# Performance work log

Measured on AMD Instinct MI355X. Metric: run time of the kernel, lower is better.

## Reference

```python
import jax, jax.numpy as jnp
import numpy as np

B, LQ, LK, D, H = 4, 1024, 2048, 1024, 16
DH = D // H  # 64
EPS = 1e-6
ROPE_BASE = 10000.0


def _rms_norm(x, w):
    # RMSNorm over last dim (d_head)
    var = jnp.mean(jnp.square(x), axis=-1, keepdims=True)
    return x * jax.lax.rsqrt(var + EPS) * w


def _rope(x, pos):
    # x: [B,H,L,dh], pos: [L] int. Half-split rotation.
    half = x.shape[-1] // 2
    inv_freq = ROPE_BASE ** (-jnp.arange(0, half, dtype=jnp.float32) / half)
    ang = pos.astype(jnp.float32)[:, None] * inv_freq  # [L, half]
    cos, sin = jnp.cos(ang), jnp.sin(ang)              # [L, half]
    x1, x2 = x[..., :half], x[..., half:]
    return jnp.concatenate([x1 * cos - x2 * sin, x1 * sin + x2 * cos], axis=-1)


def setup_inputs() -> dict:
    key = jax.random.key(0)
    ks = jax.random.split(key, 7)
    s = 1.0 / np.sqrt(D)
    return {
        "queries": jax.random.normal(ks[0], (B, LQ, D), jnp.float32),
        "kv": jax.random.normal(ks[1], (B, LK, D), jnp.float32),
        "wq": jax.random.normal(ks[2], (D, D), jnp.float32) * s,
        "wkv": jax.random.normal(ks[3], (2 * D, D), jnp.float32) * s,
        "wo": jax.random.normal(ks[4], (D, D), jnp.float32) * s,
        "q_norm_w": jnp.ones((DH,), jnp.float32),
        "k_norm_w": jnp.ones((DH,), jnp.float32),
        "pos_q": jnp.arange(LQ, dtype=jnp.int32),
        "pos_k": jnp.arange(LK, dtype=jnp.int32),
    }


def reference(queries, kv, wq, wkv, wo, q_norm_w, k_norm_w, pos_q, pos_k):
    b, lq, d = queries.shape
    lk = kv.shape[1]
    scale = DH ** -0.5
    # projections (torch Linear: x @ W.T)
    q = (queries @ wq.T).reshape(b, lq, H, DH).transpose(0, 2, 1, 3)  # [B,H,Lq,dh]
    kvp = (kv @ wkv.T).reshape(b, lk, H, 2 * DH).transpose(0, 2, 1, 3)
    k, v = kvp[..., :DH], kvp[..., DH:]                               # [B,H,Lk,dh]
    q = _rms_norm(q, q_norm_w)
    k = _rms_norm(k, k_norm_w)
    q = _rope(q, pos_q)
    k = _rope(k, pos_k)
    scores = jnp.einsum("bhqd,bhkd->bhqk", q, k) * scale
    attn = jax.nn.softmax(scores, axis=-1)
    y = jnp.einsum("bhqk,bhkd->bhqd", attn, v)        # [B,H,Lq,dh]
    y = y.transpose(0, 2, 1, 3).reshape(b, lq, d)     # [B,Lq,D]
    return y @ wo.T
```

## Files before the change

kernel.cpp:

```cpp
#include <hip/hip_runtime.h>
#include <stdint.h>

typedef unsigned short u16;
typedef u16 u16x8 __attribute__((ext_vector_type(8)));
typedef u16 u16x4 __attribute__((ext_vector_type(4)));
typedef short s16x8 __attribute__((ext_vector_type(8)));
typedef float f32x4 __attribute__((ext_vector_type(4)));

#define B_ 4
#define LQ_ 1024
#define LK_ 2048
#define D_ 1024
#define H_ 16
#define DH_ 64
#define QSCL 0.1803368801111204f
#define L2_10000 13.287712379549449f

__device__ __forceinline__ u16 f2bf(float x) {
  uint32_t u = __float_as_uint(x);
  u += 0x7FFFu + ((u >> 16) & 1u);
  return (u16)(u >> 16);
}
__device__ __forceinline__ float bf2f(u16 h) {
  return __uint_as_float(((uint32_t)h) << 16);
}
__device__ __forceinline__ uint32_t cvtpk(float lo, float hi) {
  uint32_t r;
  asm("v_cvt_pk_bf16_f32 %0, %1, %2" : "=v"(r) : "v"(lo), "v"(hi));
  return r;
}
__device__ __forceinline__ float exp2fast(float x) {
  float r;
  asm("v_exp_f32 %0, %1" : "=v"(r) : "v"(x));
  return r;
}

__global__ __launch_bounds__(256) void castw_k(const float* __restrict__ src,
                                               u16* __restrict__ dst, int n) {
  int i = (blockIdx.x * 256 + threadIdx.x) * 4;
  if (i >= n) return;
  float4 v = *(const float4*)(src + i);
  ushort4 o;
  o.x = f2bf(v.x); o.y = f2bf(v.y); o.z = f2bf(v.z); o.w = f2bf(v.w);
  *(ushort4*)(dst + i) = o;
}

__global__ __launch_bounds__(256) void gemm_bt(const u16* __restrict__ A,
                                               const u16* __restrict__ Bm,
                                               float* __restrict__ C,
                                               int N) {
  __shared__ __align__(16) u16 As[2][128 * 32];
  __shared__ __align__(16) u16 Bs[2][128 * 32];
  const int tid = threadIdx.x;
  const int lane = tid & 63;
  const int wid = tid >> 6;
  const int m0 = blockIdx.x * 128;
  const int n0 = blockIdx.y * 128;
  const int slice = 1024 / gridDim.z;
  const int kStart = blockIdx.z * slice;
  const int NT = slice >> 5;
  C += (size_t)blockIdx.z * (size_t)gridDim.x * 128 * N;
  const int wr = (wid >> 1) * 64;
  const int wc = (wid & 1) * 64;
  const int fr = lane & 15;
  const int fq = lane >> 4;
  const int srow = lane >> 2;
  const int schunk = lane & 3;

  f32x4 zero = {0.f, 0.f, 0.f, 0.f};
  f32x4 acc[4][4];
  for (int i = 0; i < 4; i++)
    for (int j = 0; j < 4; j++) acc[i][j] = zero;

  const int r0 = wid * 32;
  const u16* gA = A + (size_t)(m0 + r0 + srow) * 1024 + schunk * 8;
  const u16* gB = Bm + (size_t)(n0 + r0 + srow) * 1024 + schunk * 8;

  auto stage = [&](int buf, int k0) {
    u16* lA = &As[buf][r0 * 32];
    u16* lB = &Bs[buf][r0 * 32];
    __builtin_amdgcn_global_load_lds(
        (const __attribute__((address_space(1))) void*)(gA + k0),
        (__attribute__((address_space(3))) void*)(lA), 16, 0, 0);
    __builtin_amdgcn_global_load_lds(
        (const __attribute__((address_space(1))) void*)(gA + k0 + (size_t)16 * 1024),
        (__attribute__((address_space(3))) void*)(lA + 16 * 32), 16, 0, 0);
    __builtin_amdgcn_global_load_lds(
        (const __attribute__((address_space(1))) void*)(gB + k0),
        (__attribute__((address_space(3))) void*)(lB), 16, 0, 0);
    __builtin_amdgcn_global_load_lds(
        (const __attribute__((address_space(1))) void*)(gB + k0 + (size_t)16 * 1024),
        (__attribute__((address_space(3))) void*)(lB + 16 * 32), 16, 0, 0);
  };

  stage(0, kStart);
  stage(1, kStart + 32);
  asm volatile("s_waitcnt vmcnt(4)" ::: "memory");
  __builtin_amdgcn_s_barrier();

  for (int t = 0; t < NT; t++) {
    const int cur = t & 1;
    s16x8 af[4], bf[4];
#pragma unroll
    for (int mi = 0; mi < 4; mi++)
      af[mi] = *(const s16x8*)&As[cur][(wr + mi * 16 + fr) * 32 + fq * 8];
#pragma unroll
    for (int ni = 0; ni < 4; ni++)
      bf[ni] = *(const s16x8*)&Bs[cur][(wc + ni * 16 + fr) * 32 + fq * 8];
#pragma unroll
    for (int mi = 0; mi < 4; mi++)
#pragma unroll
      for (int ni = 0; ni < 4; ni++)
        acc[mi][ni] = __builtin_amdgcn_mfma_f32_16x16x32_bf16(af[mi], bf[ni],
                                                              acc[mi][ni], 0, 0, 0);
    __builtin_amdgcn_s_barrier();
    if (t + 2 < NT) {
      stage(cur, kStart + (t + 2) * 32);
      asm volatile("s_waitcnt vmcnt(4)" ::: "memory");
    } else {
      asm volatile("s_waitcnt vmcnt(0)" ::: "memory");
    }
    __builtin_amdgcn_s_barrier();
  }
#pragma unroll
  for (int mi = 0; mi < 4; mi++) {
#pragma unroll
    for (int ni = 0; ni < 4; ni++) {
      int row = m0 + wr + mi * 16 + fq * 4;
      int col = n0 + wc + ni * 16 + fr;
#pragma unroll
      for (int r = 0; r < 4; r++) C[(size_t)(row + r) * N + col] = acc[mi][ni][r];
    }
  }
}

#define BAR8 asm volatile("s_barrier" ::: "memory")
__global__ __launch_bounds__(512, 2) void gemm_bt256(const u16* __restrict__ A,
                                                     const u16* __restrict__ Bm,
                                                     u16* __restrict__ C) {
  __shared__ __align__(16) u16 lds[65536];
  const int N = 2048;
  const int tid = threadIdx.x;
  const int lane = tid & 63;
  const int w = tid >> 6;
  const int wr = w >> 2;
  const int wc = w & 3;
  const int fr = lane & 15;
  const int fq = lane >> 4;
  const int nwg = gridDim.x;
  const int cpx = nwg >> 3;
  const int bid = blockIdx.x;
  const int swz = (bid & 7) * cpx + (bid >> 3);
  const int nbn = N >> 8;
  const int bm = swz / nbn, bn = swz % nbn;
  const int gm0 = bm * 256, gn0 = bn * 256;
  const int NT = 16;

  f32x4 zero = {0.f, 0.f, 0.f, 0.f};
  f32x4 acc[8][4];
#pragma unroll
  for (int i = 0; i < 8; i++)
#pragma unroll
    for (int j = 0; j < 4; j++) acc[i][j] = zero;

  auto stage = [&](int buf, int t, int s) {
    int q = (s & 3) * 512 + tid;
    int row = q >> 3, p = q & 7;
    int l = p ^ (row & 7);
    const u16* src = (s < 4)
        ? A + (size_t)(gm0 + row) * 1024 + (t << 6) + l * 8
        : Bm + (size_t)(gn0 + row) * 1024 + (t << 6) + l * 8;
    u16* dst = &lds[buf * 32768 + ((s < 4) ? 0 : 16384) + ((s & 3) * 512 + w * 64) * 8];
    __builtin_amdgcn_global_load_lds(
        (const __attribute__((address_space(1))) void*)src,
        (__attribute__((address_space(3))) void*)dst, 16, 0, 0);
  };
  auto rdA = [&](int buf, int mi, int kk) -> s16x8 {
    int row = wr * 128 + mi * 16 + fr;
    int l = (kk * 4 + fq) ^ (fr & 7);
    return *(const s16x8*)&lds[buf * 32768 + row * 64 + l * 8];
  };
  auto rdB = [&](int buf, int ni, int kk) -> s16x8 {
    int row = wc * 64 + ni * 16 + fr;
    int l = (kk * 4 + fq) ^ (fr & 7);
    return *(const s16x8*)&lds[buf * 32768 + 16384 + row * 64 + l * 8];
  };

  s16x8 af[4][2], bf[4][2];

#pragma unroll
  for (int s = 4; s < 8; s++) stage(0, 0, s);
#pragma unroll
  for (int s = 0; s < 4; s++) stage(0, 0, s);
#pragma unroll
  for (int s = 4; s < 8; s++) stage(1, 1, s);
#pragma unroll
  for (int s = 0; s < 4; s++) stage(1, 1, s);
  asm volatile("s_waitcnt vmcnt(8)" ::: "memory");
  BAR8;

  for (int t = 0; t < NT; t++) {
    const int cur = t & 1;
    const bool st2 = (t + 2 < NT);
#pragma unroll
    for (int mi = 0; mi < 4; mi++)
#pragma unroll
      for (int kk = 0; kk < 2; kk++) af[mi][kk] = rdA(cur, mi, kk);
#pragma unroll
    for (int ni = 0; ni < 2; ni++)
#pragma unroll
      for (int kk = 0; kk < 2; kk++) bf[ni][kk] = rdB(cur, ni, kk);
    BAR8;
    __builtin_amdgcn_s_setprio(1);
#pragma unroll
    for (int mi = 0; mi < 4; mi++)
#pragma unroll
      for (int ni = 0; ni < 2; ni++)
#pragma unroll
        for (int kk = 0; kk < 2; kk++)
          acc[mi][ni] = __builtin_amdgcn_mfma_f32_16x16x32_bf16(af[mi][kk], bf[ni][kk],
                                                                acc[mi][ni], 0, 0, 0);
    __builtin_amdgcn_s_setprio(0);
    BAR8;
#pragma unroll
    for (int ni = 2; ni < 4; ni++)
#pragma unroll
      for (int kk = 0; kk < 2; kk++) bf[ni][kk] = rdB(cur, ni, kk);
    BAR8;
    __builtin_amdgcn_s_setprio(1);
#pragma unroll
    for (int mi = 0; mi < 4; mi++)
#pragma unroll
      for (int ni = 2; ni < 4; ni++)
#pragma unroll
        for (int kk = 0; kk < 2; kk++)
          acc[mi][ni] = __builtin_amdgcn_mfma_f32_16x16x32_bf16(af[mi][kk], bf[ni][kk],
                                                                acc[mi][ni], 0, 0, 0);
    __builtin_amdgcn_s_setprio(0);
    BAR8;
#pragma unroll
    for (int mi = 0; mi < 4; mi++)
#pragma unroll
      for (int kk = 0; kk < 2; kk++) af[mi][kk] = rdA(cur, mi + 4, kk);
    if (st2) {
#pragma unroll
      for (int s = 4; s < 8; s++) stage(cur, t + 2, s);
    }
    BAR8;
    __builtin_amdgcn_s_setprio(1);
#pragma unroll
    for (int mi = 0; mi < 4; mi++)
#pragma unroll
      for (int ni = 2; ni < 4; ni++)
#pragma unroll
        for (int kk = 0; kk < 2; kk++)
          acc[mi + 4][ni] = __builtin_amdgcn_mfma_f32_16x16x32_bf16(
              af[mi][kk], bf[ni][kk], acc[mi + 4][ni], 0, 0, 0);
    __builtin_amdgcn_s_setprio(0);
    BAR8;
    if (st2) {
#pragma unroll
      for (int s = 0; s < 4; s++) stage(cur, t + 2, s);
      asm volatile("s_waitcnt vmcnt(8)" ::: "memory");
    } else {
      asm volatile("s_waitcnt vmcnt(0)" ::: "memory");
    }
    BAR8;
    __builtin_amdgcn_s_setprio(1);
#pragma unroll
    for (int mi = 0; mi < 4; mi++)
#pragma unroll
      for (int ni = 0; ni < 2; ni++)
#pragma unroll
        for (int kk = 0; kk < 2; kk++)
          acc[mi + 4][ni] = __builtin_amdgcn_mfma_f32_16x16x32_bf16(
              af[mi][kk], bf[ni][kk], acc[mi + 4][ni], 0, 0, 0);
    __builtin_amdgcn_s_setprio(0);
    BAR8;
  }
#pragma unroll
  for (int mi = 0; mi < 8; mi++) {
#pragma unroll
    for (int ni = 0; ni < 4; ni++) {
      int row = gm0 + wr * 128 + mi * 16 + fq * 4;
      int col = gn0 + wc * 64 + ni * 16 + fr;
#pragma unroll
      for (int r = 0; r < 4; r++) C[(size_t)(row + r) * N + col] = f2bf(acc[mi][ni][r]);
    }
  }
}

__global__ __launch_bounds__(256) void norm_rope_q(const float* __restrict__ src,
                                                   size_t partStride,
                                                   const float* __restrict__ w,
                                                   const int* __restrict__ pos,
                                                   u16* __restrict__ dst) {
  int wid = threadIdx.x >> 6;
  int lane = threadIdx.x & 63;
  int g = blockIdx.x * 4 + wid;
  int h = g & 15;
  int bl = g >> 4;
  int b = bl >> 10;
  int l = bl & 1023;
  size_t idx = (size_t)bl * 1024 + h * 64 + lane;
  float x = src[idx] + src[partStride + idx];
  float ss = x * x;
#pragma unroll
  for (int m = 1; m < 64; m <<= 1) ss += __shfl_xor(ss, m, 64);
  float xn = x * rsqrtf(ss * (1.0f / 64.0f) + 1e-6f) * w[lane];
  float p = __shfl_xor(xn, 32, 64);
  int j = lane & 31;
  float freq = exp2fast(-(float)j * (L2_10000 / 32.f));
  float ang = (float)pos[l] * freq;
  float c = cosf(ang), s = sinf(ang);
  float o = (lane < 32) ? (xn * c - p * s) : (p * s + xn * c);
  dst[((size_t)(b * 16 + h) * 1024 + l) * 64 + lane] = f2bf(o * QSCL);
}

__global__ __launch_bounds__(256) void norm_rope_kv(const u16* __restrict__ src,
                                                    const float* __restrict__ w,
                                                    const int* __restrict__ pos,
                                                    u16* __restrict__ dst) {
  int wid = threadIdx.x >> 6;
  int lane = threadIdx.x & 63;
  int g = blockIdx.x * 4 + wid;
  int h = g & 15;
  int bl = g >> 4;
  int b = bl >> 11;
  int l = bl & 2047;
  float x = bf2f(src[(size_t)bl * 2048 + h * 128 + lane]);
  float ss = x * x;
#pragma unroll
  for (int m = 1; m < 64; m <<= 1) ss += __shfl_xor(ss, m, 64);
  float xn = x * rsqrtf(ss * (1.0f / 64.0f) + 1e-6f) * w[lane];
  float p = __shfl_xor(xn, 32, 64);
  int j = lane & 31;
  float freq = exp2fast(-(float)j * (L2_10000 / 32.f));
  float ang = (float)pos[l] * freq;
  float c = cosf(ang), s = sinf(ang);
  float o = (lane < 32) ? (xn * c - p * s) : (p * s + xn * c);
  dst[((size_t)(b * 16 + h) * 2048 + l) * 64 + lane] = f2bf(o);
}

__global__ __launch_bounds__(256) void reduce2_k(const float* __restrict__ p,
                                                 float* __restrict__ out, int n) {
  int i = (blockIdx.x * 256 + threadIdx.x) * 4;
  if (i >= n) return;
  float4 a = *(const float4*)(p + i);
  float4 b = *(const float4*)(p + (size_t)n + i);
  float4 r = make_float4(a.x + b.x, a.y + b.y, a.z + b.z, a.w + b.w);
  *(float4*)(out + i) = r;
}

__global__ __launch_bounds__(256) void vtrans_k(const u16* __restrict__ kvp,
                                                u16* __restrict__ vt) {
  __shared__ u16 tile[64][66];
  int kt = blockIdx.x & 31;
  int bh = blockIdx.x >> 5;
  int h = bh & 15;
  int b = bh >> 4;
  int c = threadIdx.x & 63;
  int r4 = threadIdx.x >> 6;
  const u16* src = kvp + ((size_t)(b * LK_ + kt * 64)) * 2048 + h * 128 + 64;
#pragma unroll
  for (int p = 0; p < 16; p++) {
    int lk = p * 4 + r4;
    tile[lk][c] = src[(size_t)lk * 2048 + c];
  }
  __syncthreads();
  u16* dst = vt + (size_t)bh * 64 * LK_ + kt * 64;
#pragma unroll
  for (int p = 0; p < 16; p++) {
    int dh = p * 4 + r4;
    dst[(size_t)dh * LK_ + c] = tile[c][dh];
  }
}

__global__ __launch_bounds__(256) void flash_k(const u16* __restrict__ qb,
                                               const u16* __restrict__ kb,
                                               const u16* __restrict__ vb,
                                               u16* __restrict__ y1) {
  __shared__ __align__(16) u16 Ks[2][64][64];
  __shared__ __align__(16) u16 Vs[2][64][64];
  const int tid = threadIdx.x;
  const int lane = tid & 63;
  const int wid = tid >> 6;
  const int fr = lane & 15;
  const int fq = lane >> 4;
  int bid = blockIdx.x;
  int vbid = (bid & 7) * 64 + (bid >> 3);
  int qt = vbid & 7;
  int bh = vbid >> 3;
  const u16* qbase = qb + ((size_t)bh * LQ_ + qt * 128 + wid * 32) * 64;
  const u16* kbase = kb + (size_t)bh * LK_ * 64;
  const u16* vbase = vb + (size_t)bh * 64 * LK_;
  s16x8 qf0a = *(const s16x8*)(qbase + (size_t)fr * 64 + fq * 8);
  s16x8 qf1a = *(const s16x8*)(qbase + (size_t)fr * 64 + 32 + fq * 8);
  s16x8 qf0b = *(const s16x8*)(qbase + (size_t)(16 + fr) * 64 + fq * 8);
  s16x8 qf1b = *(const s16x8*)(qbase + (size_t)(16 + fr) * 64 + 32 + fq * 8);
  float mrunA = -1e30f, lrunA = 0.f;
  float mrunB = -1e30f, lrunB = 0.f;
  f32x4 zero = {0.f, 0.f, 0.f, 0.f};
  f32x4 yaccA[4], yaccB[4];
#pragma unroll
  for (int ni = 0; ni < 4; ni++) { yaccA[ni] = zero; yaccB[ni] = zero; }
  const int srow = tid >> 3;
  const int schunk = tid & 7;
  const int c2 = schunk >> 2, c1 = (schunk >> 1) & 1, c0 = schunk & 1;
  const int vg1 = 4 * c2 + 2 * c0;
  const int voff = 4 * c1;

  auto kaddr = [&](int bufi, int row) -> u16* {
    return &Ks[bufi][row][(schunk ^ (row & 7)) << 3];
  };
  auto stageV = [&](int bufi, int row, u16x8 v) {
    u16x4 lo4 = __builtin_shufflevector(v, v, 0, 1, 2, 3);
    u16x4 hi4 = __builtin_shufflevector(v, v, 4, 5, 6, 7);
    *(u16x4*)&Vs[bufi][row][((vg1 ^ (row & 7)) << 3) + voff] = lo4;
    *(u16x4*)&Vs[bufi][row][(((vg1 + 1) ^ (row & 7)) << 3) + voff] = hi4;
  };
  auto qk2 = [&](int bufi, f32x4 (&sA)[4], f32x4 (&sB)[4]) {
#pragma unroll
    for (int ni = 0; ni < 4; ni++) { sA[ni] = zero; sB[ni] = zero; }
#pragma unroll
    for (int ni = 0; ni < 4; ni++) {
      int row = ni * 16 + fr;
      s16x8 kf0 = *(const s16x8*)&Ks[bufi][row][(fq ^ (fr & 7)) << 3];
      s16x8 kf1 = *(const s16x8*)&Ks[bufi][row][((4 + fq) ^ (fr & 7)) << 3];
      sA[ni] = __builtin_amdgcn_mfma_f32_16x16x32_bf16(kf0, qf0a, sA[ni], 0, 0, 0);
      sA[ni] = __builtin_amdgcn_mfma_f32_16x16x32_bf16(kf1, qf1a, sA[ni], 0, 0, 0);
      sB[ni] = __builtin_amdgcn_mfma_f32_16x16x32_bf16(kf0, qf0b, sB[ni], 0, 0, 0);
      sB[ni] = __builtin_amdgcn_mfma_f32_16x16x32_bf16(kf1, qf1b, sB[ni], 0, 0, 0);
    }
  };
  auto softmax = [&](f32x4 (&sp)[4], float& mrun, float& lrun, f32x4 (&yacc)[4]) {
    float m0 = fmaxf(fmaxf(sp[0][0], sp[0][1]), sp[0][2]);
    float m1 = fmaxf(fmaxf(sp[0][3], sp[1][0]), sp[1][1]);
    float m2 = fmaxf(fmaxf(sp[1][2], sp[1][3]), sp[2][0]);
    float m3 = fmaxf(fmaxf(sp[2][1], sp[2][2]), sp[2][3]);
    float m4 = fmaxf(fmaxf(sp[3][0], sp[3][1]), sp[3][2]);
    float mx = fmaxf(fmaxf(fmaxf(m0, m1), m2), fmaxf(fmaxf(m3, m4), sp[3][3]));
    mx = fmaxf(mx, __shfl_xor(mx, 16, 64));
    mx = fmaxf(mx, __shfl_xor(mx, 32, 64));
    bool skip = __all(mx <= mrun + 10.0f);
    float ts = 0.f;
    if (!skip) {
      float mn = fmaxf(mrun, mx);
      float alpha = exp2fast(mrun - mn);
      mrun = mn;
      float va[4];
#pragma unroll
      for (int r = 0; r < 4; r++) va[r] = __shfl(alpha, fq * 4 + r, 64);
#pragma unroll
      for (int ni = 0; ni < 4; ni++)
#pragma unroll
        for (int r = 0; r < 4; r++) yacc[ni][r] *= va[r];
      lrun *= alpha;
    }
#pragma unroll
    for (int ni = 0; ni < 4; ni++)
#pragma unroll
      for (int r = 0; r < 4; r++) {
        float pv = exp2fast(sp[ni][r] - mrun);
        sp[ni][r] = pv;
        ts += pv;
      }
    ts += __shfl_xor(ts, 16, 64);
    ts += __shfl_xor(ts, 32, 64);
    lrun += ts;
  };

  const int NT = LK_ / 64;
  f32x4 spA[4], spB[4], snA[4], snB[4];

  {
    u16x8 k0 = *(const u16x8*)(kbase + (size_t)srow * 64 + schunk * 8);
    u16x8 k1 = *(const u16x8*)(kbase + (size_t)(srow + 32) * 64 + schunk * 8);
    u16x8 v0 = *(const u16x8*)(vbase + (size_t)srow * LK_ + schunk * 8);
    u16x8 v1 = *(const u16x8*)(vbase + (size_t)(srow + 32) * LK_ + schunk * 8);
    *(u16x8*)kaddr(0, srow) = k0;
    *(u16x8*)kaddr(0, srow + 32) = k1;
    stageV(0, srow, v0);
    stageV(0, srow + 32, v1);
    __syncthreads();
    u16x8 ka = *(const u16x8*)(kbase + (size_t)(64 + srow) * 64 + schunk * 8);
    u16x8 kb2 = *(const u16x8*)(kbase + (size_t)(64 + srow + 32) * 64 + schunk * 8);
    u16x8 va = *(const u16x8*)(vbase + (size_t)srow * LK_ + 64 + schunk * 8);
    u16x8 vb2 = *(const u16x8*)(vbase + (size_t)(srow + 32) * LK_ + 64 + schunk * 8);
    *(u16x8*)kaddr(1, srow) = ka;
    *(u16x8*)kaddr(1, srow + 32) = kb2;
    stageV(1, srow, va);
    stageV(1, srow + 32, vb2);
    qk2(0, spA, spB);
    __syncthreads();
  }

  for (int t = 0; t < NT; t++) {
    const int cur = t & 1;
    const bool st2 = (t + 2 < NT);
    u16x8 kr0, kr1, vr0, vr1;
    if (st2) {
      int kt = (t + 2) * 64;
      kr0 = *(const u16x8*)(kbase + (size_t)(kt + srow) * 64 + schunk * 8);
      kr1 = *(const u16x8*)(kbase + (size_t)(kt + srow + 32) * 64 + schunk * 8);
      vr0 = *(const u16x8*)(vbase + (size_t)srow * LK_ + kt + schunk * 8);
      vr1 = *(const u16x8*)(vbase + (size_t)(srow + 32) * LK_ + kt + schunk * 8);
    }
    if (t + 1 < NT) qk2(cur ^ 1, snA, snB);
    softmax(spA, mrunA, lrunA, yaccA);
    softmax(spB, mrunB, lrunB, yaccB);
#pragma unroll
    for (int s2 = 0; s2 < 2; s2++) {
      union { uint32_t u[4]; s16x8 v8; } puA, puB;
      puA.u[0] = cvtpk(spA[2 * s2][0], spA[2 * s2][1]);
      puA.u[1] = cvtpk(spA[2 * s2][2], spA[2 * s2][3]);
      puA.u[2] = cvtpk(spA[2 * s2 + 1][0], spA[2 * s2 + 1][1]);
      puA.u[3] = cvtpk(spA[2 * s2 + 1][2], spA[2 * s2 + 1][3]);
      puB.u[0] = cvtpk(spB[2 * s2][0], spB[2 * s2][1]);
      puB.u[1] = cvtpk(spB[2 * s2][2], spB[2 * s2][3]);
      puB.u[2] = cvtpk(spB[2 * s2 + 1][0], spB[2 * s2 + 1][1]);
      puB.u[3] = cvtpk(spB[2 * s2 + 1][2], spB[2 * s2 + 1][3]);
#pragma unroll
      for (int ni = 0; ni < 4; ni++) {
        int row = ni * 16 + fr;
        s16x8 vf = *(const s16x8*)&Vs[cur][row][(((4 * s2 + fq) ^ (fr & 7)) << 3)];
        yaccA[ni] = __builtin_amdgcn_mfma_f32_16x16x32_bf16(puA.v8, vf, yaccA[ni], 0, 0, 0);
        yaccB[ni] = __builtin_amdgcn_mfma_f32_16x16x32_bf16(puB.v8, vf, yaccB[ni], 0, 0, 0);
      }
    }
    __syncthreads();
    if (st2) {
      *(u16x8*)kaddr(cur, srow) = kr0;
      *(u16x8*)kaddr(cur, srow + 32) = kr1;
      stageV(cur, srow, vr0);
      stageV(cur, srow + 32, vr1);
    }
    __syncthreads();
#pragma unroll
    for (int ni = 0; ni < 4; ni++) { spA[ni] = snA[ni]; spB[ni] = snB[ni]; }
  }
  int b = bh >> 4, h = bh & 15;
  float lrA[4], lrB[4];
#pragma unroll
  for (int r = 0; r < 4; r++) {
    lrA[r] = __shfl(lrunA, fq * 4 + r, 64);
    lrB[r] = __shfl(lrunB, fq * 4 + r, 64);
  }
  u16* yoA = y1 + ((size_t)(b * LQ_ + qt * 128 + wid * 32 + fq * 4)) * 1024 + h * 64;
  u16* yoB = yoA + (size_t)16 * 1024;
#pragma unroll
  for (int ni = 0; ni < 4; ni++) {
#pragma unroll
    for (int r = 0; r < 4; r++) {
      yoA[(size_t)r * 1024 + ni * 16 + fr] = f2bf(yaccA[ni][r] / lrA[r]);
      yoB[(size_t)r * 1024 + ni * 16 + fr] = f2bf(yaccB[ni][r] / lrB[r]);
    }
  }
}

extern "C" void kernel_launch(void* const* d_in, const int* in_sizes, int n_in,
                              void* d_out, int out_size, void* d_ws, size_t ws_size,
                              hipStream_t stream) {
  (void)in_sizes; (void)n_in; (void)out_size;
  const float* queries = (const float*)d_in[0];
  const float* kv = (const float*)d_in[1];
  const float* wq = (const float*)d_in[2];
  const float* wkv = (const float*)d_in[3];
  const float* wo = (const float*)d_in[4];
  const float* qnw = (const float*)d_in[5];
  const float* knw = (const float*)d_in[6];
  const int* pos_q = (const int*)d_in[7];
  const int* pos_k = (const int*)d_in[8];
  float* out = (float*)d_out;

  char* ws = (char*)d_ws;
  size_t off = 0;
  auto alloc = [&](size_t sz) { void* p = ws + off; off += sz; return p; };
  u16* Aq1 = (u16*)alloc((size_t)4096 * 1024 * 2);
  u16* Wqh = (u16*)alloc((size_t)1024 * 1024 * 2);
  u16* Akv1 = (u16*)alloc((size_t)8192 * 1024 * 2);
  u16* Wkvh = (u16*)alloc((size_t)2048 * 1024 * 2);
  u16* Woh = (u16*)alloc((size_t)1024 * 1024 * 2);
  u16* KVp = (u16*)alloc((size_t)8192 * 2048 * 2);
  u16* Qb = (u16*)alloc((size_t)64 * 1024 * 64 * 2);
  u16* Kb = (u16*)alloc((size_t)64 * 2048 * 64 * 2);
  u16* Vt = (u16*)alloc((size_t)64 * 2048 * 64 * 2);
  u16* Y1 = (u16*)alloc((size_t)4096 * 1024 * 2);
  float* Part = (float*)alloc((size_t)2 * 4096 * 1024 * 4);
  if (off > ws_size) return;

  const size_t PSTRIDE = (size_t)4096 * 1024;

  castw_k<<<4096 * 1024 / 1024, 256, 0, stream>>>(queries, Aq1, 4096 * 1024);
  castw_k<<<1024 * 1024 / 1024, 256, 0, stream>>>(wq, Wqh, 1024 * 1024);
  castw_k<<<8192 * 1024 / 1024, 256, 0, stream>>>(kv, Akv1, 8192 * 1024);
  castw_k<<<2048 * 1024 / 1024, 256, 0, stream>>>(wkv, Wkvh, 2048 * 1024);
  castw_k<<<1024 * 1024 / 1024, 256, 0, stream>>>(wo, Woh, 1024 * 1024);
  gemm_bt256<<<(8192 / 256) * (2048 / 256), 512, 0, stream>>>(Akv1, Wkvh, KVp);
  gemm_bt<<<dim3(4096 / 128, 1024 / 128, 2), 256, 0, stream>>>(Aq1, Wqh, Part, 1024);
  norm_rope_q<<<4096 * 16 / 4, 256, 0, stream>>>(Part, PSTRIDE, qnw, pos_q, Qb);
  norm_rope_kv<<<8192 * 16 / 4, 256, 0, stream>>>(KVp, knw, pos_k, Kb);
  vtrans_k<<<64 * 32, 256, 0, stream>>>(KVp, Vt);
  flash_k<<<64 * 8, 256, 0, stream>>>(Qb, Kb, Vt, Y1);
  gemm_bt<<<dim3(4096 / 128, 1024 / 128, 2), 256, 0, stream>>>(Y1, Woh, Part, 1024);
  reduce2_k<<<4096, 256, 0, stream>>>(Part, out, 4096 * 1024);
}
```

Before: 207.3 us.

## Fuse K norm-rope with V transpose; compute softmax row sums via MFMA

Merges the K RMSNorm+RoPE kernel and the V transpose kernel into a single launch that processes one 64-row tile of K and V per block. This removes one launch and lets both parts share the block's indexing. In the flash kernel, the per-row softmax denominator is no longer built from exp sums and cross-lane shuffles. Instead, an extra MFMA multiplies the bf16 probabilities by a ones vector, which adds MFMA work but removes VALU adds and shuffles; the denominator now sums bf16-rounded probabilities rather than fp32 ones.

```diff
diff --git a/kernel.cpp b/kernel.cpp
--- a/kernel.cpp
+++ b/kernel.cpp
@@ -317,29 +317,49 @@
   dst[((size_t)(b * 16 + h) * 1024 + l) * 64 + lane] = f2bf(o * QSCL);
 }
 
-__global__ __launch_bounds__(256) void norm_rope_kv(const u16* __restrict__ src,
-                                                    const float* __restrict__ w,
-                                                    const int* __restrict__ pos,
-                                                    u16* __restrict__ dst) {
-  int wid = threadIdx.x >> 6;
-  int lane = threadIdx.x & 63;
-  int g = blockIdx.x * 4 + wid;
-  int h = g & 15;
-  int bl = g >> 4;
-  int b = bl >> 11;
-  int l = bl & 2047;
-  float x = bf2f(src[(size_t)bl * 2048 + h * 128 + lane]);
-  float ss = x * x;
-#pragma unroll
-  for (int m = 1; m < 64; m <<= 1) ss += __shfl_xor(ss, m, 64);
-  float xn = x * rsqrtf(ss * (1.0f / 64.0f) + 1e-6f) * w[lane];
-  float p = __shfl_xor(xn, 32, 64);
-  int j = lane & 31;
-  float freq = exp2fast(-(float)j * (L2_10000 / 32.f));
-  float ang = (float)pos[l] * freq;
-  float c = cosf(ang), s = sinf(ang);
-  float o = (lane < 32) ? (xn * c - p * s) : (p * s + xn * c);
-  dst[((size_t)(b * 16 + h) * 2048 + l) * 64 + lane] = f2bf(o);
+__global__ __launch_bounds__(256) void normv_k(const u16* __restrict__ src,
+                                               const float* __restrict__ w,
+                                               const int* __restrict__ pos,
+                                               u16* __restrict__ Kb,
+                                               u16* __restrict__ Vt) {
+  __shared__ u16 tile[64][66];
+  int kt = blockIdx.x & 31;
+  int bh = blockIdx.x >> 5;
+  int h = bh & 15;
+  int b = bh >> 4;
+  int c = threadIdx.x & 63;
+  int r4 = threadIdx.x >> 6;
+  const u16* ksrc = src + ((size_t)(b * LK_ + kt * 64)) * 2048 + h * 128;
+  u16* kdst = Kb + ((size_t)bh * LK_ + kt * 64) * 64;
+  float wn = w[c];
+  float freq = exp2fast(-(float)(c & 31) * (L2_10000 / 32.f));
+#pragma unroll
+  for (int p = 0; p < 16; p++) {
+    int lk = p * 4 + r4;
+    float x = bf2f(ksrc[(size_t)lk * 2048 + c]);
+    float ss = x * x;
+#pragma unroll
+    for (int m = 1; m < 64; m <<= 1) ss += __shfl_xor(ss, m, 64);
+    float xn = x * rsqrtf(ss * (1.0f / 64.0f) + 1e-6f) * wn;
+    float pv = __shfl_xor(xn, 32, 64);
+    float ang = (float)pos[kt * 64 + lk] * freq;
+    float cc = cosf(ang), s = sinf(ang);
+    float o = (c < 32) ? (xn * cc - pv * s) : (pv * s + xn * cc);
+    kdst[(size_t)lk * 64 + c] = f2bf(o);
+  }
+  const u16* vsrc = ksrc + 64;
+#pragma unroll
+  for (int p = 0; p < 16; p++) {
+    int lk = p * 4 + r4;
+    tile[lk][c] = vsrc[(size_t)lk * 2048 + c];
+  }
+  __syncthreads();
+  u16* vdst = Vt + (size_t)bh * 64 * LK_ + kt * 64;
+#pragma unroll
+  for (int p = 0; p < 16; p++) {
+    int dh = p * 4 + r4;
+    vdst[(size_t)dh * LK_ + c] = tile[c][dh];
+  }
 }
 
 __global__ __launch_bounds__(256) void reduce2_k(const float* __restrict__ p,
@@ -350,30 +370,6 @@
   float4 b = *(const float4*)(p + (size_t)n + i);
   float4 r = make_float4(a.x + b.x, a.y + b.y, a.z + b.z, a.w + b.w);
   *(float4*)(out + i) = r;
-}
-
-__global__ __launch_bounds__(256) void vtrans_k(const u16* __restrict__ kvp,
-                                                u16* __restrict__ vt) {
-  __shared__ u16 tile[64][66];
-  int kt = blockIdx.x & 31;
-  int bh = blockIdx.x >> 5;
-  int h = bh & 15;
-  int b = bh >> 4;
-  int c = threadIdx.x & 63;
-  int r4 = threadIdx.x >> 6;
-  const u16* src = kvp + ((size_t)(b * LK_ + kt * 64)) * 2048 + h * 128 + 64;
-#pragma unroll
-  for (int p = 0; p < 16; p++) {
-    int lk = p * 4 + r4;
-    tile[lk][c] = src[(size_t)lk * 2048 + c];
-  }
-  __syncthreads();
-  u16* dst = vt + (size_t)bh * 64 * LK_ + kt * 64;
-#pragma unroll
-  for (int p = 0; p < 16; p++) {
-    int dh = p * 4 + r4;
-    dst[(size_t)dh * LK_ + c] = tile[c][dh];
-  }
 }
 
 __global__ __launch_bounds__(256) void flash_k(const u16* __restrict__ qb,
@@ -398,10 +394,12 @@
   s16x8 qf1a = *(const s16x8*)(qbase + (size_t)fr * 64 + 32 + fq * 8);
   s16x8 qf0b = *(const s16x8*)(qbase + (size_t)(16 + fr) * 64 + fq * 8);
   s16x8 qf1b = *(const s16x8*)(qbase + (size_t)(16 + fr) * 64 + 32 + fq * 8);
-  float mrunA = -1e30f, lrunA = 0.f;
-  float mrunB = -1e30f, lrunB = 0.f;
+  s16x8 ones;
+#pragma unroll
+  for (int e = 0; e < 8; e++) ones[e] = (short)0x3F80;
+  float mrunA = -1e30f, mrunB = -1e30f;
   f32x4 zero = {0.f, 0.f, 0.f, 0.f};
-  f32x4 yaccA[4], yaccB[4];
+  f32x4 yaccA[4], yaccB[4], yonesA = zero, yonesB = zero;
 #pragma unroll
   for (int ni = 0; ni < 4; ni++) { yaccA[ni] = zero; yaccB[ni] = zero; }
   const int srow = tid >> 3;
@@ -433,7 +431,7 @@
       sB[ni] = __builtin_amdgcn_mfma_f32_16x16x32_bf16(kf1, qf1b, sB[ni], 0, 0, 0);
     }
   };
-  auto softmax = [&](f32x4 (&sp)[4], float& mrun, float& lrun, f32x4 (&yacc)[4]) {
+  auto softmax = [&](f32x4 (&sp)[4], float& mrun, f32x4 (&yacc)[4], f32x4& yones) {
     float m0 = fmaxf(fmaxf(sp[0][0], sp[0][1]), sp[0][2]);
     float m1 = fmaxf(fmaxf(sp[0][3], sp[1][0]), sp[1][1]);
     float m2 = fmaxf(fmaxf(sp[1][2], sp[1][3]), sp[2][0]);
@@ -443,7 +441,6 @@
     mx = fmaxf(mx, __shfl_xor(mx, 16, 64));
     mx = fmaxf(mx, __shfl_xor(mx, 32, 64));
     bool skip = __all(mx <= mrun + 10.0f);
-    float ts = 0.f;
     if (!skip) {
       float mn = fmaxf(mrun, mx);
       float alpha = exp2fast(mrun - mn);
@@ -455,19 +452,13 @@
       for (int ni = 0; ni < 4; ni++)
 #pragma unroll
         for (int r = 0; r < 4; r++) yacc[ni][r] *= va[r];
-      lrun *= alpha;
+#pragma unroll
+      for (int r = 0; r < 4; r++) yones[r] *= va[r];
     }
 #pragma unroll
     for (int ni = 0; ni < 4; ni++)
 #pragma unroll
-      for (int r = 0; r < 4; r++) {
-        float pv = exp2fast(sp[ni][r] - mrun);
-        sp[ni][r] = pv;
-        ts += pv;
-      }
-    ts += __shfl_xor(ts, 16, 64);
-    ts += __shfl_xor(ts, 32, 64);
-    lrun += ts;
+      for (int r = 0; r < 4; r++) sp[ni][r] = exp2fast(sp[ni][r] - mrun);
   };
 
   const int NT = LK_ / 64;
@@ -507,8 +498,8 @@
       vr1 = *(const u16x8*)(vbase + (size_t)(srow + 32) * LK_ + kt + schunk * 8);
     }
     if (t + 1 < NT) qk2(cur ^ 1, snA, snB);
-    softmax(spA, mrunA, lrunA, yaccA);
-    softmax(spB, mrunB, lrunB, yaccB);
+    softmax(spA, mrunA, yaccA, yonesA);
+    softmax(spB, mrunB, yaccB, yonesB);
 #pragma unroll
     for (int s2 = 0; s2 < 2; s2++) {
       union { uint32_t u[4]; s16x8 v8; } puA, puB;
@@ -527,6 +518,8 @@
         yaccA[ni] = __builtin_amdgcn_mfma_f32_16x16x32_bf16(puA.v8, vf, yaccA[ni], 0, 0, 0);
         yaccB[ni] = __builtin_amdgcn_mfma_f32_16x16x32_bf16(puB.v8, vf, yaccB[ni], 0, 0, 0);
       }
+      yonesA = __builtin_amdgcn_mfma_f32_16x16x32_bf16(puA.v8, ones, yonesA, 0, 0, 0);
+      yonesB = __builtin_amdgcn_mfma_f32_16x16x32_bf16(puB.v8, ones, yonesB, 0, 0, 0);
     }
     __syncthreads();
     if (st2) {
@@ -540,20 +533,14 @@
     for (int ni = 0; ni < 4; ni++) { spA[ni] = snA[ni]; spB[ni] = snB[ni]; }
   }
   int b = bh >> 4, h = bh & 15;
-  float lrA[4], lrB[4];
-#pragma unroll
-  for (int r = 0; r < 4; r++) {
-    lrA[r] = __shfl(lrunA, fq * 4 + r, 64);
-    lrB[r] = __shfl(lrunB, fq * 4 + r, 64);
-  }
   u16* yoA = y1 + ((size_t)(b * LQ_ + qt * 128 + wid * 32 + fq * 4)) * 1024 + h * 64;
   u16* yoB = yoA + (size_t)16 * 1024;
 #pragma unroll
   for (int ni = 0; ni < 4; ni++) {
 #pragma unroll
     for (int r = 0; r < 4; r++) {
-      yoA[(size_t)r * 1024 + ni * 16 + fr] = f2bf(yaccA[ni][r] / lrA[r]);
-      yoB[(size_t)r * 1024 + ni * 16 + fr] = f2bf(yaccB[ni][r] / lrB[r]);
+      yoA[(size_t)r * 1024 + ni * 16 + fr] = f2bf(yaccA[ni][r] / yonesA[r]);
+      yoB[(size_t)r * 1024 + ni * 16 + fr] = f2bf(yaccB[ni][r] / yonesB[r]);
     }
   }
 }
@@ -599,8 +586,7 @@
   gemm_bt256<<<(8192 / 256) * (2048 / 256), 512, 0, stream>>>(Akv1, Wkvh, KVp);
   gemm_bt<<<dim3(4096 / 128, 1024 / 128, 2), 256, 0, stream>>>(Aq1, Wqh, Part, 1024);
   norm_rope_q<<<4096 * 16 / 4, 256, 0, stream>>>(Part, PSTRIDE, qnw, pos_q, Qb);
-  norm_rope_kv<<<8192 * 16 / 4, 256, 0, stream>>>(KVp, knw, pos_k, Kb);
-  vtrans_k<<<64 * 32, 256, 0, stream>>>(KVp, Vt);
+  normv_k<<<64 * 32, 256, 0, stream>>>(KVp, knw, pos_k, Kb, Vt);
   flash_k<<<64 * 8, 256, 0, stream>>>(Qb, Kb, Vt, Y1);
   gemm_bt<<<dim3(4096 / 128, 1024 / 128, 2), 256, 0, stream>>>(Y1, Woh, Part, 1024);
   reduce2_k<<<4096, 256, 0, stream>>>(Part, out, 4096 * 1024);
```

New measurement: 199.8 us. 3.6% less time.
